# Kernel tuning notes

Hardware: AMD Instinct MI355X
Metric: run time of the kernel (lower is better)

The kernel has to match this reference:

```python
import jax, jax.numpy as jnp
import numpy as np

TOP_K = 8
NUM_EXPERTS = 256
NUM_GROUPS = 8
TOPK_GROUP = 4
SCALE = 2.5
EPS = 1e-20


def setup_inputs() -> dict:
    key = jax.random.key(0)
    k1, k2, k3 = jax.random.split(key, 3)
    T, H = 8192, 7168
    hidden_states = jax.random.normal(k1, (T, H), dtype=jnp.float32)
    # scale ~ kaiming-ish so logits are O(1) and sigmoid is not saturated
    weight = jax.random.normal(k2, (NUM_EXPERTS, H), dtype=jnp.float32) * (H ** -0.5)
    e_score_correction_bias = jax.random.normal(k3, (NUM_EXPERTS,), dtype=jnp.float32) * 0.1
    return {"hidden_states": hidden_states, "weight": weight,
            "e_score_correction_bias": e_score_correction_bias}


def reference(hidden_states, weight, e_score_correction_bias):
    T = hidden_states.shape[0]
    epg = NUM_EXPERTS // NUM_GROUPS  # experts per group
    # gating logits: [T, E]
    logits = jnp.einsum('th,eh->te', hidden_states.astype(jnp.float32),
                        weight.astype(jnp.float32))
    scores = jax.nn.sigmoid(logits)
    scores_for_choice = scores + e_score_correction_bias[None, :]
    # group score = sum of top-2 corrected scores within each group: [T, G]
    grouped = scores_for_choice.reshape(T, NUM_GROUPS, epg)
    top2, _ = jax.lax.top_k(grouped, 2)
    group_scores = top2.sum(axis=-1)
    # select topk_group groups, build mask [T, G]
    _, group_idx = jax.lax.top_k(group_scores, TOPK_GROUP)
    group_mask = jnp.zeros((T, NUM_GROUPS), dtype=scores.dtype)
    group_mask = group_mask.at[jnp.arange(T)[:, None], group_idx].set(1.0)
    # expand to expert mask [T, E]
    score_mask = jnp.repeat(group_mask, epg, axis=1)
    tmp_scores = jnp.where(score_mask > 0, scores_for_choice, 0.0)
    # top_k experts among allowed groups
    _, topk_idx = jax.lax.top_k(tmp_scores, TOP_K)
    # gather UNcorrected scores as weights
    topk_weight = jnp.take_along_axis(scores, topk_idx, axis=1)
    topk_weight = topk_weight / (topk_weight.sum(axis=-1, keepdims=True) + EPS)
    topk_weight = topk_weight * SCALE
    return topk_idx, topk_weight
```

## Files before the change

### kernel.cpp

```cpp
#include <hip/hip_runtime.h>
#include <cmath>

typedef __attribute__((ext_vector_type(8))) _Float16 half8;
typedef __attribute__((ext_vector_type(8))) unsigned short ushort8;
typedef __attribute__((ext_vector_type(4))) float f32x4;

#define HH 7168
#define NE 256
#define NQ 224
#define NWND 56
#define TOPK 8
#define TOPKG 4
#define WSC 1024.f
#define INV_WS (1.f/1024.f)
#define C1 (1.f/2048.f)
#define C2 (1.f/4194304.f)

__device__ __forceinline__ void split2(float x, unsigned short& h, unsigned short& m){
  const _Float16 hh = (_Float16)x;
  const float r = x - (float)hh;
  const _Float16 mm = (_Float16)(r * 2048.f);
  h = __builtin_bit_cast(unsigned short, hh);
  m = __builtin_bit_cast(unsigned short, mm);
}

__global__ __launch_bounds__(256) void prep_w(const float* __restrict__ wgt,
                                              unsigned short* __restrict__ bh,
                                              unsigned short* __restrict__ bm){
  const int b = blockIdx.x;
  const int nt = b & 15, qb = (b >> 4) * 4;
  const int w = threadIdx.x >> 6, L = threadIdx.x & 63;
  const int q = qb + w;
  const int e = nt*16 + (L & 15);
  const int k0 = 32*q + 8*(L >> 4);
  const float4 a0 = *(const float4*)(wgt + (size_t)e*HH + k0);
  const float4 a1 = *(const float4*)(wgt + (size_t)e*HH + k0 + 4);
  const float v[8] = {a0.x,a0.y,a0.z,a0.w,a1.x,a1.y,a1.z,a1.w};
  ushort8 h8, m8;
#pragma unroll
  for(int j=0;j<8;j++){ unsigned short hh,mm; split2(v[j]*WSC, hh, mm); h8[j]=hh; m8[j]=mm; }
  const size_t base = ((size_t)(q*16+nt)*64 + L)*8;
  *(ushort8*)(bh+base) = h8;
  *(ushort8*)(bm+base) = m8;
}

#define AB(aw,lvl,mt,q,row) (((((aw)*4+(lvl)*2+(mt))*4+(q))*64+(row))*16)
__device__ __forceinline__ int swz(int bo){ return bo ^ (((bo >> 8) & 7) << 4); }

__device__ __forceinline__ void glds16(const void* g, void* l){
  __builtin_amdgcn_global_load_lds(
      (const __attribute__((address_space(1))) unsigned int*)g,
      (__attribute__((address_space(3))) unsigned int*)l, 16, 0, 0);
}

#define BAR_V4  do{ asm volatile("s_waitcnt vmcnt(4)" ::: "memory"); __builtin_amdgcn_s_barrier(); __builtin_amdgcn_sched_barrier(0); }while(0)
#define BAR_V2  do{ asm volatile("s_waitcnt vmcnt(2)" ::: "memory"); __builtin_amdgcn_s_barrier(); __builtin_amdgcn_sched_barrier(0); }while(0)
#define BAR_V2L do{ asm volatile("s_waitcnt lgkmcnt(0)\n\ts_waitcnt vmcnt(2)" ::: "memory"); __builtin_amdgcn_s_barrier(); __builtin_amdgcn_sched_barrier(0); }while(0)
#define BAR_V0  do{ asm volatile("s_waitcnt vmcnt(0)" ::: "memory"); __builtin_amdgcn_s_barrier(); __builtin_amdgcn_sched_barrier(0); }while(0)

#define KAHAN do{ \
  _Pragma("unroll") \
  for(int cc=0;cc<2;cc++) \
    _Pragma("unroll") \
    for(int r=0;r<4;r++){ \
      const float v = c0[cc][r] + c1[cc][r]*C1 + c2[cc][r]*C2; \
      const float y = v - kcmp[cc][r]; \
      const float t = ksum[cc][r] + y; \
      kcmp[cc][r] = (t - ksum[cc][r]) - y; \
      ksum[cc][r] = t; \
    } \
}while(0)

__global__ __launch_bounds__(512,4)
void gemm(const float* __restrict__ hs,
          const unsigned short* __restrict__ bhp,
          const unsigned short* __restrict__ bmp,
          float* __restrict__ lgout){
  __shared__ __align__(16) unsigned char blds[49152];
  __shared__ __align__(16) unsigned char alds[32768];

  const int tid = threadIdx.x, lane = tid & 63, w = tid >> 6;
  const int b = blockIdx.x;
  const int slice = (b >> 2) & 1;
  const int tg = (b >> 3)*4 + (b & 3);
  const int tb = tg*32, eb = slice*128;
  const int mtp = w >> 2, ntp = w & 3;

  f32x4 ksum[2], kcmp[2], c0[2], c1[2], c2[2];
#pragma unroll
  for(int cc=0;cc<2;cc++){ ksum[cc]=f32x4{0,0,0,0}; kcmp[cc]=f32x4{0,0,0,0}; }

  const int tokS = tid >> 4, kidx = tid & 15;
  const int mtS = tokS >> 4, m16S = tokS & 15;
  const int qS = kidx >> 2, kgS = kidx & 3;
  const int rowS = kgS*16 + m16S;
  const float* agp = hs + (size_t)(tb + tokS)*HH + kidx*8;
  float4 ga[2];

  auto stage = [&](int aw){
    unsigned short h[8], m[8];
    const float* gv = (const float*)ga;
#pragma unroll
    for(int p=0;p<8;p++) split2(gv[p], h[p], m[p]);
    ushort8 h8, m8;
#pragma unroll
    for(int j=0;j<8;j++){ h8[j]=h[j]; m8[j]=m[j]; }
    *(ushort8*)&alds[swz(AB(aw,0,mtS,qS,rowS))] = h8;
    *(ushort8*)&alds[swz(AB(aw,1,mtS,qS,rowS))] = m8;
  };

  const unsigned short* bsrc = (w >= 4 ? bmp : bhp)
      + ((size_t)((slice*8 + (w&3)*2)*64 + lane))*8;
  const int bdst = (w>>2)*8192 + (w&3)*2048;
  auto issueB = [&](int bufoff, int qpre){
    const unsigned short* s0 = bsrc + (size_t)qpre*8192;
    glds16(s0,       &blds[bufoff + bdst]);
    glds16(s0 + 512, &blds[bufoff + bdst + 1024]);
  };

  auto compute = [&](int awr, int q, int bc){
    const half8 ah = *(const half8*)&alds[swz(AB(awr,0,mtp,q,lane))];
    const half8 am = *(const half8*)&alds[swz(AB(awr,1,mtp,q,lane))];
    half8 Bh[2], Bm[2];
#pragma unroll
    for(int ntl=0;ntl<2;ntl++){
      Bh[ntl] = *(const half8*)&blds[bc + (ntp*2+ntl)*1024 + lane*16];
      Bm[ntl] = *(const half8*)&blds[bc + 8192 + (ntp*2+ntl)*1024 + lane*16];
    }
    __builtin_amdgcn_s_setprio(1);
#pragma unroll
    for(int ntl=0;ntl<2;ntl++){
      c0[ntl] = __builtin_amdgcn_mfma_f32_16x16x32_f16(ah, Bh[ntl], c0[ntl], 0,0,0);
      c1[ntl] = __builtin_amdgcn_mfma_f32_16x16x32_f16(ah, Bm[ntl], c1[ntl], 0,0,0);
      c1[ntl] = __builtin_amdgcn_mfma_f32_16x16x32_f16(am, Bh[ntl], c1[ntl], 0,0,0);
      c2[ntl] = __builtin_amdgcn_mfma_f32_16x16x32_f16(am, Bm[ntl], c2[ntl], 0,0,0);
    }
    __builtin_amdgcn_s_setprio(0);
  };

  ga[0] = *(const float4*)agp; ga[1] = *(const float4*)(agp+4);
  issueB(0,     0);
  issueB(16384, 1);
  stage(0);
  asm volatile("s_waitcnt lgkmcnt(0)\n\ts_waitcnt vmcnt(2)" ::: "memory");
  __builtin_amdgcn_s_barrier();
  __builtin_amdgcn_sched_barrier(0);

  int bc = 0;
#pragma unroll 1
  for(int wnd=0; wnd<NWND-1; ++wnd){
    const int i0 = wnd*4;
    const int awr = wnd & 1, aws = awr ^ 1;
    int bp;
    bp = bc + 32768; if(bp >= 49152) bp -= 49152;
    issueB(bp, i0+2);
    { const float* ap = agp + (size_t)(wnd+1)*128;
      ga[0] = *(const float4*)ap; ga[1] = *(const float4*)(ap+4); }
#pragma unroll
    for(int cc=0;cc<2;cc++){ c0[cc]=f32x4{0,0,0,0}; c1[cc]=f32x4{0,0,0,0}; c2[cc]=f32x4{0,0,0,0}; }
    compute(awr, 0, bc);
    BAR_V4;
    bc += 16384; if(bc == 49152) bc = 0;
    bp = bc + 32768; if(bp >= 49152) bp -= 49152;
    issueB(bp, i0+3);
    compute(awr, 1, bc);
    BAR_V4;
    bc += 16384; if(bc == 49152) bc = 0;
    bp = bc + 32768; if(bp >= 49152) bp -= 49152;
    issueB(bp, i0+4);
    compute(awr, 2, bc);
    stage(aws);
    BAR_V2L;
    bc += 16384; if(bc == 49152) bc = 0;
    bp = bc + 32768; if(bp >= 49152) bp -= 49152;
    issueB(bp, i0+5);
    compute(awr, 3, bc);
    KAHAN;
    BAR_V2;
    bc += 16384; if(bc == 49152) bc = 0;
  }
  {
    int bp;
    bp = bc + 32768; if(bp >= 49152) bp -= 49152;
    issueB(bp, 222);
#pragma unroll
    for(int cc=0;cc<2;cc++){ c0[cc]=f32x4{0,0,0,0}; c1[cc]=f32x4{0,0,0,0}; c2[cc]=f32x4{0,0,0,0}; }
    compute(1, 0, bc);
    BAR_V2;
    bc += 16384; if(bc == 49152) bc = 0;
    bp = bc + 32768; if(bp >= 49152) bp -= 49152;
    issueB(bp, 223);
    compute(1, 1, bc);
    BAR_V2;
    bc += 16384; if(bc == 49152) bc = 0;
    compute(1, 2, bc);
    BAR_V0;
    bc += 16384; if(bc == 49152) bc = 0;
    compute(1, 3, bc);
    KAHAN;
  }

#pragma unroll
  for(int ntl=0;ntl<2;ntl++)
#pragma unroll
    for(int r=0;r<4;r++){
      const int tok = mtp*16 + (lane>>4)*4 + r;
      const int e = (ntp*2+ntl)*16 + (lane&15);
      const float lg = (ksum[ntl][r] - kcmp[ntl][r]) * INV_WS;
      lgout[(size_t)(tb+tok)*NE + eb + e] = lg;
    }
}

__global__ __launch_bounds__(256)
void gate(const float* __restrict__ lg, const float* __restrict__ bias,
          float* __restrict__ out, int T){
  const int tid = threadIdx.x, lane = tid & 63, wv = tid >> 6;
  const int t = blockIdx.x*4 + wv;
  const float4 bias4 = *(const float4*)(bias + 4*lane);
  const int g = lane >> 3;
  const float NEG_INF = -__builtin_inff();

  const float4 l4 = *(const float4*)(lg + (size_t)t*NE + 4*lane);
  float4 r4;
  r4.x = 1.f/(1.f + expf(-l4.x));
  r4.y = 1.f/(1.f + expf(-l4.y));
  r4.z = 1.f/(1.f + expf(-l4.z));
  r4.w = 1.f/(1.f + expf(-l4.w));
  float4 s4;
  s4.x = r4.x + bias4.x; s4.y = r4.y + bias4.y;
  s4.z = r4.z + bias4.z; s4.w = r4.w + bias4.w;

  float m1 = s4.x, m2 = NEG_INF;
  if (s4.y > m1) { m2 = m1; m1 = s4.y; } else if (s4.y > m2) m2 = s4.y;
  if (s4.z > m1) { m2 = m1; m1 = s4.z; } else if (s4.z > m2) m2 = s4.z;
  if (s4.w > m1) { m2 = m1; m1 = s4.w; } else if (s4.w > m2) m2 = s4.w;
#pragma unroll
  for (int m = 1; m <= 4; m <<= 1) {
    const float o1 = __shfl_xor(m1, m);
    const float o2 = __shfl_xor(m2, m);
    const float nm1 = fmaxf(m1, o1);
    const float nm2 = fmaxf(fminf(m1, o1), fmaxf(m2, o2));
    m1 = nm1; m2 = nm2;
  }
  const float gs = m1 + m2;

  float gsv[8];
#pragma unroll
  for (int j = 0; j < 8; ++j) gsv[j] = __shfl(gs, j * 8);

  unsigned gm = 0;
#pragma unroll
  for (int r = 0; r < TOPKG; ++r) {
    float best = NEG_INF; int bj = 0;
#pragma unroll
    for (int j = 0; j < 8; ++j) {
      const bool avail = !((gm >> j) & 1u);
      if (avail && gsv[j] > best) { best = gsv[j]; bj = j; }
    }
    gm |= 1u << bj;
  }
  const bool allowed = (gm >> g) & 1u;

  float v0 = allowed ? s4.x : 0.f;
  float v1 = allowed ? s4.y : 0.f;
  float v2 = allowed ? s4.z : 0.f;
  float v3 = allowed ? s4.w : 0.f;

  float sumw = 0.f;
  int myidx = 0; float myraw = 0.f;
#pragma unroll
  for (int r = 0; r < TOPK; ++r) {
    float bv = v0; int bj = 0;
    if (v1 > bv) { bv = v1; bj = 1; }
    if (v2 > bv) { bv = v2; bj = 2; }
    if (v3 > bv) { bv = v3; bj = 3; }
    int bidx = 4 * lane + bj;
#pragma unroll
    for (int m = 1; m < 64; m <<= 1) {
      const float ov = __shfl_xor(bv, m);
      const int   oi = __shfl_xor(bidx, m);
      if (ov > bv || (ov == bv && oi < bidx)) { bv = ov; bidx = oi; }
    }
    const int oj = bidx & 3;
    const float cand = (oj == 0) ? r4.x
                     : (oj == 1) ? r4.y
                     : (oj == 2) ? r4.z
                     :             r4.w;
    const float raw = __shfl(cand, bidx >> 2);
    sumw += raw;
    if (lane == r) { myidx = bidx; myraw = raw; }
    if (lane == (bidx >> 2)) {
      if      (oj == 0) v0 = NEG_INF;
      else if (oj == 1) v1 = NEG_INF;
      else if (oj == 2) v2 = NEG_INF;
      else              v3 = NEG_INF;
    }
  }

  if (lane < TOPK) {
    out[(size_t)t * TOPK + lane] = (float)myidx;
    out[(size_t)T * TOPK + (size_t)t * TOPK + lane] = myraw / (sumw + 1e-20f) * 2.5f;
  }
}

extern "C" void kernel_launch(void* const* d_in, const int* in_sizes, int n_in,
                              void* d_out, int out_size, void* d_ws, size_t ws_size,
                              hipStream_t stream) {
  const float* hs   = (const float*)d_in[0];
  const float* wgt  = (const float*)d_in[1];
  const float* bias = (const float*)d_in[2];
  float* out = (float*)d_out;

  const int T = in_sizes[0] / HH;

  unsigned short* bh = (unsigned short*)d_ws;
  unsigned short* bm = bh + (size_t)NE*HH;
  float* lgbuf = (float*)(bm + (size_t)NE*HH);

  hipLaunchKernelGGL(prep_w, dim3(896), dim3(256), 0, stream, wgt, bh, bm);
  hipLaunchKernelGGL(gemm,   dim3(512), dim3(512), 0, stream, hs, bh, bm, lgbuf);
  hipLaunchKernelGGL(gate,   dim3(T/4), dim3(256), 0, stream, lgbuf, bias, out, T);
}
```

Measured before the change: 456.8 us.

## Deepen B-operand LDS ring to six slots and halve barriers per window

Doubles the LDS ring for the split-fp16 weight tiles from three to six 16 KB slots, so four K-steps are in flight. Each four-step window now has two barriers instead of four, and B prefetches are issued two steps at a time. The separate tail iteration is folded into the main loop behind a `more` flag. This aims to cut barrier stalls and hide global-to-LDS latency, but the larger LDS footprint (128 KB per block) and the lowered launch-bounds occupancy hint leave fewer resident blocks per CU.

```diff
diff --git a/kernel.cpp b/kernel.cpp
--- a/kernel.cpp
+++ b/kernel.cpp
@@ -9,6 +9,7 @@
 #define NE 256
 #define NQ 224
 #define NWND 56
+#define NITER 112
 #define TOPK 8
 #define TOPKG 4
 #define WSC 1024.f
@@ -53,11 +54,6 @@
       (__attribute__((address_space(3))) unsigned int*)l, 16, 0, 0);
 }
 
-#define BAR_V4  do{ asm volatile("s_waitcnt vmcnt(4)" ::: "memory"); __builtin_amdgcn_s_barrier(); __builtin_amdgcn_sched_barrier(0); }while(0)
-#define BAR_V2  do{ asm volatile("s_waitcnt vmcnt(2)" ::: "memory"); __builtin_amdgcn_s_barrier(); __builtin_amdgcn_sched_barrier(0); }while(0)
-#define BAR_V2L do{ asm volatile("s_waitcnt lgkmcnt(0)\n\ts_waitcnt vmcnt(2)" ::: "memory"); __builtin_amdgcn_s_barrier(); __builtin_amdgcn_sched_barrier(0); }while(0)
-#define BAR_V0  do{ asm volatile("s_waitcnt vmcnt(0)" ::: "memory"); __builtin_amdgcn_s_barrier(); __builtin_amdgcn_sched_barrier(0); }while(0)
-
 #define KAHAN do{ \
   _Pragma("unroll") \
   for(int cc=0;cc<2;cc++) \
@@ -71,12 +67,12 @@
     } \
 }while(0)
 
-__global__ __launch_bounds__(512,4)
+__global__ __launch_bounds__(512,2)
 void gemm(const float* __restrict__ hs,
           const unsigned short* __restrict__ bhp,
           const unsigned short* __restrict__ bmp,
           float* __restrict__ lgout){
-  __shared__ __align__(16) unsigned char blds[49152];
+  __shared__ __align__(16) unsigned char blds[98304];
   __shared__ __align__(16) unsigned char alds[32768];
 
   const int tid = threadIdx.x, lane = tid & 63, w = tid >> 6;
@@ -112,20 +108,20 @@
   const unsigned short* bsrc = (w >= 4 ? bmp : bhp)
       + ((size_t)((slice*8 + (w&3)*2)*64 + lane))*8;
   const int bdst = (w>>2)*8192 + (w&3)*2048;
-  auto issueB = [&](int bufoff, int qpre){
-    const unsigned short* s0 = bsrc + (size_t)qpre*8192;
-    glds16(s0,       &blds[bufoff + bdst]);
-    glds16(s0 + 512, &blds[bufoff + bdst + 1024]);
+  auto issueB = [&](int slotoff, int q32){
+    const unsigned short* s0 = bsrc + (size_t)q32*8192;
+    glds16(s0,       &blds[slotoff + bdst]);
+    glds16(s0 + 512, &blds[slotoff + bdst + 1024]);
   };
 
-  auto compute = [&](int awr, int q, int bc){
-    const half8 ah = *(const half8*)&alds[swz(AB(awr,0,mtp,q,lane))];
-    const half8 am = *(const half8*)&alds[swz(AB(awr,1,mtp,q,lane))];
+  auto compute = [&](int awr, int qloc, int bco){
+    const half8 ah = *(const half8*)&alds[swz(AB(awr,0,mtp,qloc,lane))];
+    const half8 am = *(const half8*)&alds[swz(AB(awr,1,mtp,qloc,lane))];
     half8 Bh[2], Bm[2];
 #pragma unroll
     for(int ntl=0;ntl<2;ntl++){
-      Bh[ntl] = *(const half8*)&blds[bc + (ntp*2+ntl)*1024 + lane*16];
-      Bm[ntl] = *(const half8*)&blds[bc + 8192 + (ntp*2+ntl)*1024 + lane*16];
+      Bh[ntl] = *(const half8*)&blds[bco + (ntp*2+ntl)*1024 + lane*16];
+      Bm[ntl] = *(const half8*)&blds[bco + 8192 + (ntp*2+ntl)*1024 + lane*16];
     }
     __builtin_amdgcn_s_setprio(1);
 #pragma unroll
@@ -141,63 +137,52 @@
   ga[0] = *(const float4*)agp; ga[1] = *(const float4*)(agp+4);
   issueB(0,     0);
   issueB(16384, 1);
+  issueB(32768, 2);
+  issueB(49152, 3);
   stage(0);
-  asm volatile("s_waitcnt lgkmcnt(0)\n\ts_waitcnt vmcnt(2)" ::: "memory");
+  asm volatile("s_waitcnt vmcnt(4) lgkmcnt(0)" ::: "memory");
   __builtin_amdgcn_s_barrier();
-  __builtin_amdgcn_sched_barrier(0);
-
-  int bc = 0;
+
+  int sA = 0;
 #pragma unroll 1
-  for(int wnd=0; wnd<NWND-1; ++wnd){
-    const int i0 = wnd*4;
-    const int awr = wnd & 1, aws = awr ^ 1;
-    int bp;
-    bp = bc + 32768; if(bp >= 49152) bp -= 49152;
-    issueB(bp, i0+2);
-    { const float* ap = agp + (size_t)(wnd+1)*128;
-      ga[0] = *(const float4*)ap; ga[1] = *(const float4*)(ap+4); }
+  for(int wnd=0; wnd<NWND; ++wnd){
+    const int awr = wnd & 1;
+    const int s0 = sA;
+    const int s1 = s0+1;
+    int s2 = s0+2; if(s2>=6) s2-=6;
+    int s3 = s2+1;
+    int s4 = s2+2; if(s4>=6) s4-=6;
+    int s5 = s4+1;
+    const int q0 = 4*wnd;
+    const bool more = (wnd+1 < NWND);
+
+    if(more){
+      const float* ap = agp + (size_t)(wnd+1)*128;
+      ga[0] = *(const float4*)ap; ga[1] = *(const float4*)(ap+4);
+      issueB(s4*16384, q0+4);
+      issueB(s5*16384, q0+5);
+    }
 #pragma unroll
     for(int cc=0;cc<2;cc++){ c0[cc]=f32x4{0,0,0,0}; c1[cc]=f32x4{0,0,0,0}; c2[cc]=f32x4{0,0,0,0}; }
-    compute(awr, 0, bc);
-    BAR_V4;
-    bc += 16384; if(bc == 49152) bc = 0;
-    bp = bc + 32768; if(bp >= 49152) bp -= 49152;
-    issueB(bp, i0+3);
-    compute(awr, 1, bc);
-    BAR_V4;
-    bc += 16384; if(bc == 49152) bc = 0;
-    bp = bc + 32768; if(bp >= 49152) bp -= 49152;
-    issueB(bp, i0+4);
-    compute(awr, 2, bc);
-    stage(aws);
-    BAR_V2L;
-    bc += 16384; if(bc == 49152) bc = 0;
-    bp = bc + 32768; if(bp >= 49152) bp -= 49152;
-    issueB(bp, i0+5);
-    compute(awr, 3, bc);
+    compute(awr, 0, s0*16384);
+    compute(awr, 1, s1*16384);
+    if(more){ asm volatile("s_waitcnt vmcnt(6)" ::: "memory"); }
+    else    { asm volatile("s_waitcnt vmcnt(0)" ::: "memory"); }
+    __builtin_amdgcn_s_barrier();
+
+    if(more){
+      issueB(s0*16384, q0+6);
+      issueB(s1*16384, q0+7);
+    }
+    compute(awr, 2, s2*16384);
+    compute(awr, 3, s3*16384);
+    if(more) stage(awr^1);
     KAHAN;
-    BAR_V2;
-    bc += 16384; if(bc == 49152) bc = 0;
-  }
-  {
-    int bp;
-    bp = bc + 32768; if(bp >= 49152) bp -= 49152;
-    issueB(bp, 222);
-#pragma unroll
-    for(int cc=0;cc<2;cc++){ c0[cc]=f32x4{0,0,0,0}; c1[cc]=f32x4{0,0,0,0}; c2[cc]=f32x4{0,0,0,0}; }
-    compute(1, 0, bc);
-    BAR_V2;
-    bc += 16384; if(bc == 49152) bc = 0;
-    bp = bc + 32768; if(bp >= 49152) bp -= 49152;
-    issueB(bp, 223);
-    compute(1, 1, bc);
-    BAR_V2;
-    bc += 16384; if(bc == 49152) bc = 0;
-    compute(1, 2, bc);
-    BAR_V0;
-    bc += 16384; if(bc == 49152) bc = 0;
-    compute(1, 3, bc);
-    KAHAN;
+    if(more){
+      asm volatile("s_waitcnt vmcnt(4) lgkmcnt(0)" ::: "memory");
+      __builtin_amdgcn_s_barrier();
+    }
+    sA += 4; if(sA>=6) sA-=6;
   }
 
 #pragma unroll
```

New measurement: 545.2 us. 1.19x slower.
